# Kernel tuning notes

Measured on AMD Instinct MI355X. Metric: run time of the kernel, lower is better.

## Reference

```python
import jax, jax.numpy as jnp
import numpy as np

B, DIM, SEQ = 8, 256, 16384
K, RED = 3, 3
HID = DIM // RED          # 85
PAD, STRIDE = 1, 1
EPS = 1e-5                # BatchNorm eps (inference-mode BN with running stats)


def setup_inputs() -> dict:
    key = jax.random.key(0)
    ks = jax.random.split(key, 9)
    return {
        "x": jax.random.normal(ks[0], (B, DIM, SEQ), jnp.float32),
        "w1": jax.random.normal(ks[1], (HID, DIM), jnp.float32) * 0.05,
        "bn_gamma": jax.random.uniform(ks[2], (HID,), jnp.float32, 0.5, 1.5),
        "bn_beta": jax.random.normal(ks[3], (HID,), jnp.float32) * 0.1,
        "bn_mean": jax.random.normal(ks[4], (HID,), jnp.float32) * 0.1,
        "bn_var": jax.random.uniform(ks[5], (HID,), jnp.float32, 0.5, 1.5),
        "w2": jax.random.normal(ks[6], (DIM * K, HID), jnp.float32) * 0.05,
        "b2": jax.random.normal(ks[7], (DIM * K,), jnp.float32) * 0.05,
        "bias": jax.random.normal(ks[8], (DIM,), jnp.float32) * 0.05,
    }


def reference(x, w1, bn_gamma, bn_beta, bn_mean, bn_var, w2, b2, bias):
    b = x.shape[0]
    seq = x.shape[2]
    # squeeze: adaptive avg pool over seq -> [B, DIM]
    pooled = x.mean(axis=2)
    # conv1 (1x1, no bias) + inference BatchNorm + ReLU
    y = jnp.einsum('bc,hc->bh', pooled, w1)
    y = (y - bn_mean) * (bn_gamma * jax.lax.rsqrt(bn_var + EPS)) + bn_beta
    y = jax.nn.relu(y)
    # conv2 (1x1) -> per-sample depthwise kernels [B, DIM, K]
    w = (jnp.einsum('bh,oh->bo', y, w2) + b2).reshape(b, DIM, K)
    # dynamic depthwise conv1d (emulates F.conv1d with groups = B*DIM)
    xp = jnp.pad(x, ((0, 0), (0, 0), (PAD, PAD)))
    out_len = (seq + 2 * PAD - K) // STRIDE + 1
    out = jnp.zeros((b, DIM, out_len), x.dtype)
    for kk in range(K):  # small fixed kernel loop
        out = out + w[:, :, kk:kk + 1] * xp[:, :, kk:kk + out_len * STRIDE:STRIDE]
    return out + bias[None, :, None]
```

## Files before the change

### kernel.cpp

```cpp
#include <hip/hip_runtime.h>

#define B_      8
#define DIM_    256
#define SEQ_    16384
#define K_      3
#define HID_    85
#define OUTCH_  (DIM_ * K_)
#define EPS_    1e-5f

typedef float floatx4 __attribute__((ext_vector_type(4)));

__global__ __launch_bounds__(256) void pool_kernel(const float* __restrict__ x,
                                                   float* __restrict__ pooled) {
    const int row = blockIdx.x;
    const floatx4* x4 = (const floatx4*)(x + (size_t)row * SEQ_);
    float s = 0.f;
#pragma unroll
    for (int k = 0; k < SEQ_ / 4 / 256; ++k) {
        floatx4 v = x4[threadIdx.x + k * 256];
        s += (v.x + v.y) + (v.z + v.w);
    }
#pragma unroll
    for (int off = 32; off > 0; off >>= 1) s += __shfl_down(s, off, 64);
    __shared__ float lds[4];
    const int lane = threadIdx.x & 63, wid = threadIdx.x >> 6;
    if (lane == 0) lds[wid] = s;
    __syncthreads();
    if (threadIdx.x == 0) {
        float t = (lds[0] + lds[1]) + (lds[2] + lds[3]);
        pooled[row] = t * (1.0f / SEQ_);
    }
}

__global__ __launch_bounds__(256) void conv_kernel(const float* __restrict__ x,
                                                   const float* __restrict__ pooled,
                                                   const float* __restrict__ w1,
                                                   const float* __restrict__ gamma,
                                                   const float* __restrict__ beta,
                                                   const float* __restrict__ mean,
                                                   const float* __restrict__ var,
                                                   const float* __restrict__ w2,
                                                   const float* __restrict__ b2,
                                                   const float* __restrict__ bias,
                                                   float* __restrict__ out) {
    const int row = blockIdx.x;
    const int b = row >> 8;
    const int c = row & (DIM_ - 1);

    __shared__ float sp[DIM_];
    __shared__ float sy[HID_];
    sp[threadIdx.x] = pooled[b * DIM_ + threadIdx.x];
    __syncthreads();
    if (threadIdx.x < HID_) {
        const int h = threadIdx.x;
        const float* w1r = w1 + h * DIM_;
        float acc = 0.f;
#pragma unroll 8
        for (int cc = 0; cc < DIM_; ++cc) acc = fmaf(sp[cc], w1r[cc], acc);
        float t = (acc - mean[h]) * (gamma[h] * rsqrtf(var[h] + EPS_)) + beta[h];
        sy[h] = fmaxf(t, 0.f);
    }
    __syncthreads();

    const float* w2r0 = w2 + (c * 3 + 0) * HID_;
    const float* w2r1 = w2 + (c * 3 + 1) * HID_;
    const float* w2r2 = w2 + (c * 3 + 2) * HID_;
    float w0 = b2[c * 3 + 0], w1t = b2[c * 3 + 1], w2t = b2[c * 3 + 2];
    for (int h = 0; h < HID_; ++h) {
        const float yv = sy[h];
        w0  = fmaf(yv, w2r0[h], w0);
        w1t = fmaf(yv, w2r1[h], w1t);
        w2t = fmaf(yv, w2r2[h], w2t);
    }
    const float bs = bias[c];

    const float* xr = x + (size_t)row * SEQ_;
    const floatx4* x4 = (const floatx4*)xr;
    floatx4* o4 = (floatx4*)(out + (size_t)row * SEQ_);
    const int lane = threadIdx.x & 63;
#pragma unroll
    for (int k = 0; k < SEQ_ / 4 / 256; ++k) {
        const int j = threadIdx.x + k * 256;
        const int s0 = j * 4;
        floatx4 v = x4[j];
        float left  = __shfl_up(v.w, 1, 64);
        float right = __shfl_down(v.x, 1, 64);
        if (lane == 0)  left  = (s0 > 0)        ? xr[s0 - 1] : 0.f;
        if (lane == 63) right = (s0 + 4 < SEQ_) ? xr[s0 + 4] : 0.f;
        floatx4 r;
        r.x = fmaf(w0, left, fmaf(w1t, v.x, w2t * v.y)) + bs;
        r.y = fmaf(w0, v.x,  fmaf(w1t, v.y, w2t * v.z)) + bs;
        r.z = fmaf(w0, v.y,  fmaf(w1t, v.z, w2t * v.w)) + bs;
        r.w = fmaf(w0, v.z,  fmaf(w1t, v.w, w2t * right)) + bs;
        __builtin_nontemporal_store(r, &o4[j]);
    }
}

extern "C" void kernel_launch(void* const* d_in, const int* in_sizes, int n_in,
                              void* d_out, int out_size, void* d_ws, size_t ws_size,
                              hipStream_t stream) {
    const float* x     = (const float*)d_in[0];
    const float* w1    = (const float*)d_in[1];
    const float* gamma = (const float*)d_in[2];
    const float* beta  = (const float*)d_in[3];
    const float* mean  = (const float*)d_in[4];
    const float* var   = (const float*)d_in[5];
    const float* w2    = (const float*)d_in[6];
    const float* b2    = (const float*)d_in[7];
    const float* bias  = (const float*)d_in[8];
    float* out = (float*)d_out;

    float* pooled = (float*)d_ws;

    pool_kernel<<<B_ * DIM_, 256, 0, stream>>>(x, pooled);
    conv_kernel<<<B_ * DIM_, 256, 0, stream>>>(x, pooled, w1, gamma, beta, mean,
                                               var, w2, b2, bias, out);
}
```

Baseline: 292.1 us.

## Fuse pooling and dynamic conv into one cooperative kernel with per-batch barrier

Replaces the separate pool and conv kernels with one cooperative kernel. Each block handles two channel rows, pools them, publishes the means, then spins on a per-batch atomic counter until all 256 channels of its sample are pooled. It then computes the depthwise weights and writes the conv output, rereading x while it may still sit in L2/MALL. This removes a kernel boundary and aims to cut the second HBM read of x. In exchange it adds a memset, a cooperative launch whose grid (1024 blocks) must fit co-resident, and spin-wait latency.

```diff
diff --git a/kernel.cpp b/kernel.cpp
--- a/kernel.cpp
+++ b/kernel.cpp
@@ -5,10 +5,126 @@
 #define SEQ_    16384
 #define K_      3
 #define HID_    85
-#define OUTCH_  (DIM_ * K_)
 #define EPS_    1e-5f
 
 typedef float floatx4 __attribute__((ext_vector_type(4)));
+
+__global__ __launch_bounds__(256, 4) void fused_kernel(
+        const float* __restrict__ x,
+        const float* __restrict__ w1,
+        const float* __restrict__ gamma,
+        const float* __restrict__ beta,
+        const float* __restrict__ mean,
+        const float* __restrict__ var,
+        const float* __restrict__ w2,
+        const float* __restrict__ b2,
+        const float* __restrict__ bias,
+        float* __restrict__ pooled,
+        int* __restrict__ cnt,
+        float* __restrict__ out) {
+    const int r0 = blockIdx.x * 2;
+    const int b = r0 >> 8;
+    const int c0 = r0 & (DIM_ - 1);
+    const int lane = threadIdx.x & 63, wid = threadIdx.x >> 6;
+
+    const float* xr0 = x + (size_t)r0 * SEQ_;
+    const float* xr1 = xr0 + SEQ_;
+    const floatx4* x40 = (const floatx4*)xr0;
+    const floatx4* x41 = (const floatx4*)xr1;
+
+    float s0 = 0.f, s1 = 0.f;
+#pragma unroll 4
+    for (int k = 0; k < SEQ_ / 4 / 256; ++k) {
+        floatx4 v0 = x40[threadIdx.x + k * 256];
+        floatx4 v1 = x41[threadIdx.x + k * 256];
+        s0 += (v0.x + v0.y) + (v0.z + v0.w);
+        s1 += (v1.x + v1.y) + (v1.z + v1.w);
+    }
+#pragma unroll
+    for (int off = 32; off > 0; off >>= 1) {
+        s0 += __shfl_down(s0, off, 64);
+        s1 += __shfl_down(s1, off, 64);
+    }
+    __shared__ float red0[4], red1[4];
+    if (lane == 0) { red0[wid] = s0; red1[wid] = s1; }
+    __syncthreads();
+    if (threadIdx.x == 0) {
+        pooled[r0]     = ((red0[0] + red0[1]) + (red0[2] + red0[3])) * (1.0f / SEQ_);
+        pooled[r0 + 1] = ((red1[0] + red1[1]) + (red1[2] + red1[3])) * (1.0f / SEQ_);
+        __threadfence();
+        atomicAdd(&cnt[b], 2);
+    }
+
+    if (threadIdx.x == 0) {
+        while (__hip_atomic_load(&cnt[b], __ATOMIC_ACQUIRE,
+                                 __HIP_MEMORY_SCOPE_AGENT) < DIM_)
+            __builtin_amdgcn_s_sleep(2);
+    }
+    __syncthreads();
+
+    __shared__ float sp[DIM_];
+    __shared__ float sy[HID_];
+    sp[threadIdx.x] = __hip_atomic_load(&pooled[b * DIM_ + threadIdx.x],
+                                        __ATOMIC_RELAXED, __HIP_MEMORY_SCOPE_AGENT);
+    __syncthreads();
+    if (threadIdx.x < HID_) {
+        const int h = threadIdx.x;
+        const float* w1r = w1 + h * DIM_;
+        float acc = 0.f;
+#pragma unroll 4
+        for (int cc = 0; cc < DIM_; ++cc) acc = fmaf(sp[cc], w1r[cc], acc);
+        float t = (acc - mean[h]) * (gamma[h] * rsqrtf(var[h] + EPS_)) + beta[h];
+        sy[h] = fmaxf(t, 0.f);
+    }
+    __syncthreads();
+
+    float wa0 = b2[c0 * 3 + 0], wa1 = b2[c0 * 3 + 1], wa2 = b2[c0 * 3 + 2];
+    float wb0 = b2[c0 * 3 + 3], wb1 = b2[c0 * 3 + 4], wb2 = b2[c0 * 3 + 5];
+    {
+        const float* w2r = w2 + c0 * 3 * HID_;
+        for (int h = 0; h < HID_; ++h) {
+            const float yv = sy[h];
+            wa0 = fmaf(yv, w2r[0 * HID_ + h], wa0);
+            wa1 = fmaf(yv, w2r[1 * HID_ + h], wa1);
+            wa2 = fmaf(yv, w2r[2 * HID_ + h], wa2);
+            wb0 = fmaf(yv, w2r[3 * HID_ + h], wb0);
+            wb1 = fmaf(yv, w2r[4 * HID_ + h], wb1);
+            wb2 = fmaf(yv, w2r[5 * HID_ + h], wb2);
+        }
+    }
+    const float bsa = bias[c0], bsb = bias[c0 + 1];
+
+    floatx4* o40 = (floatx4*)(out + (size_t)r0 * SEQ_);
+    floatx4* o41 = o40 + SEQ_ / 4;
+#pragma unroll 4
+    for (int k = 0; k < SEQ_ / 4 / 256; ++k) {
+        const int j = threadIdx.x + k * 256;
+        const int s0i = j * 4;
+        floatx4 v0 = x40[j];
+        floatx4 v1 = x41[j];
+        float l0 = __shfl_up(v0.w, 1, 64),  l1 = __shfl_up(v1.w, 1, 64);
+        float r0e = __shfl_down(v0.x, 1, 64), r1e = __shfl_down(v1.x, 1, 64);
+        if (lane == 0) {
+            l0 = (s0i > 0) ? xr0[s0i - 1] : 0.f;
+            l1 = (s0i > 0) ? xr1[s0i - 1] : 0.f;
+        }
+        if (lane == 63) {
+            r0e = (s0i + 4 < SEQ_) ? xr0[s0i + 4] : 0.f;
+            r1e = (s0i + 4 < SEQ_) ? xr1[s0i + 4] : 0.f;
+        }
+        floatx4 q0, q1;
+        q0.x = fmaf(wa0, l0,   fmaf(wa1, v0.x, wa2 * v0.y)) + bsa;
+        q0.y = fmaf(wa0, v0.x, fmaf(wa1, v0.y, wa2 * v0.z)) + bsa;
+        q0.z = fmaf(wa0, v0.y, fmaf(wa1, v0.z, wa2 * v0.w)) + bsa;
+        q0.w = fmaf(wa0, v0.z, fmaf(wa1, v0.w, wa2 * r0e)) + bsa;
+        q1.x = fmaf(wb0, l1,   fmaf(wb1, v1.x, wb2 * v1.y)) + bsb;
+        q1.y = fmaf(wb0, v1.x, fmaf(wb1, v1.y, wb2 * v1.z)) + bsb;
+        q1.z = fmaf(wb0, v1.y, fmaf(wb1, v1.z, wb2 * v1.w)) + bsb;
+        q1.w = fmaf(wb0, v1.z, fmaf(wb1, v1.w, wb2 * r1e)) + bsb;
+        __builtin_nontemporal_store(q0, &o40[j]);
+        __builtin_nontemporal_store(q1, &o41[j]);
+    }
+}
 
 __global__ __launch_bounds__(256) void pool_kernel(const float* __restrict__ x,
                                                    float* __restrict__ pooled) {
@@ -26,10 +142,8 @@
     const int lane = threadIdx.x & 63, wid = threadIdx.x >> 6;
     if (lane == 0) lds[wid] = s;
     __syncthreads();
-    if (threadIdx.x == 0) {
-        float t = (lds[0] + lds[1]) + (lds[2] + lds[3]);
-        pooled[row] = t * (1.0f / SEQ_);
-    }
+    if (threadIdx.x == 0)
+        pooled[row] = ((lds[0] + lds[1]) + (lds[2] + lds[3])) * (1.0f / SEQ_);
 }
 
 __global__ __launch_bounds__(256) void conv_kernel(const float* __restrict__ x,
@@ -46,7 +160,6 @@
     const int row = blockIdx.x;
     const int b = row >> 8;
     const int c = row & (DIM_ - 1);
-
     __shared__ float sp[DIM_];
     __shared__ float sy[HID_];
     sp[threadIdx.x] = pooled[b * DIM_ + threadIdx.x];
@@ -61,7 +174,6 @@
         sy[h] = fmaxf(t, 0.f);
     }
     __syncthreads();
-
     const float* w2r0 = w2 + (c * 3 + 0) * HID_;
     const float* w2r1 = w2 + (c * 3 + 1) * HID_;
     const float* w2r2 = w2 + (c * 3 + 2) * HID_;
@@ -73,7 +185,6 @@
         w2t = fmaf(yv, w2r2[h], w2t);
     }
     const float bs = bias[c];
-
     const float* xr = x + (size_t)row * SEQ_;
     const floatx4* x4 = (const floatx4*)xr;
     floatx4* o4 = (floatx4*)(out + (size_t)row * SEQ_);
@@ -110,9 +221,20 @@
     const float* bias  = (const float*)d_in[8];
     float* out = (float*)d_out;
 
-    float* pooled = (float*)d_ws;
-
-    pool_kernel<<<B_ * DIM_, 256, 0, stream>>>(x, pooled);
-    conv_kernel<<<B_ * DIM_, 256, 0, stream>>>(x, pooled, w1, gamma, beta, mean,
-                                               var, w2, b2, bias, out);
-}
+    int*   cnt    = (int*)d_ws;
+    float* pooled = (float*)d_ws + 16;
+
+    hipMemsetAsync(cnt, 0, B_ * sizeof(int), stream);
+
+    void* args[] = { (void*)&x, (void*)&w1, (void*)&gamma, (void*)&beta,
+                     (void*)&mean, (void*)&var, (void*)&w2, (void*)&b2,
+                     (void*)&bias, (void*)&pooled, (void*)&cnt, (void*)&out };
+    hipError_t e = hipLaunchCooperativeKernel((const void*)fused_kernel,
+                                              dim3(B_ * DIM_ / 2), dim3(256),
+                                              args, 0, stream);
+    if (e != hipSuccess) {
+        pool_kernel<<<B_ * DIM_, 256, 0, stream>>>(x, pooled);
+        conv_kernel<<<B_ * DIM_, 256, 0, stream>>>(x, pooled, w1, gamma, beta,
+                                                   mean, var, w2, b2, bias, out);
+    }
+}
```

After: 428.3 us. 1.47x slower.
